# Performance work log

Hardware: AMD Instinct MI355X
Metric: run time of the kernel (lower is better)

The kernel has to match this reference:

```python
import jax, jax.numpy as jnp
import numpy as np

N_NODES = 100000


def setup_inputs() -> dict:
    key = jax.random.key(0)
    k1, k2, k3, k4, k5 = jax.random.split(key, 5)
    features = jax.random.normal(k1, (N_NODES, 512), dtype=jnp.float32)
    edge_src = jax.random.randint(k2, (640000,), 0, N_NODES, dtype=jnp.int64)
    edge_dst = jax.random.randint(k3, (640000,), 0, N_NODES, dtype=jnp.int64)
    edge_weight = jax.random.uniform(k4, (640000,), dtype=jnp.float32)
    weights = jax.random.normal(k5, (512, 128), dtype=jnp.float32) * (2.0 / 512) ** 0.5  # kaiming-ish scale
    bias = jnp.zeros((128,), dtype=jnp.float32)
    return {
        "features": features,
        "edge_src": edge_src,
        "edge_dst": edge_dst,
        "edge_weight": edge_weight,
        "weights": weights,
        "bias": bias,
    }


def reference(features, edge_src, edge_dst, edge_weight, weights, bias):
    # X' = A @ (X @ W) + b, with sparse A given as COO edges (src -> dst).
    h = jnp.matmul(features, weights)                      # [N, d_out] dense GEMM
    msg = edge_weight[:, None] * h[edge_src]               # [E, d_out] gather + scale
    out = jax.ops.segment_sum(msg, edge_dst, num_segments=N_NODES)  # sparse aggregation
    return out + bias
```

## Files before the change

### kernel.cpp

```cpp
#include <hip/hip_runtime.h>


#define D_IN  512
#define D_OUT 128
#define CAP   32

typedef __attribute__((ext_vector_type(8))) short short8;
typedef __attribute__((ext_vector_type(4))) float f32x4;
typedef __attribute__((ext_vector_type(4))) int i32x4;
typedef __attribute__((ext_vector_type(8))) unsigned short u16x8;
typedef __attribute__((ext_vector_type(2))) unsigned long long u64x2;

static __device__ __forceinline__ unsigned short f2bf(float f) {
    unsigned u = __float_as_uint(f);
    unsigned r = (u + 0x7FFFu + ((u >> 16) & 1u)) >> 16;
    return (unsigned short)r;
}

static __device__ __forceinline__ int pack2(float lo, float hi) {
    return (int)((__float_as_uint(hi) & 0xFFFF0000u) | (__float_as_uint(lo) >> 16));
}

__global__ __launch_bounds__(256) void prep_kernel(const float* __restrict__ W,
                                                   unsigned short* __restrict__ Wt,
                                                   int* __restrict__ deg,
                                                   unsigned long long* __restrict__ bucket,
                                                   int M) {
    int t = blockIdx.x * 256 + threadIdx.x;
    if (t < D_OUT * D_IN) {
        int n = t >> 9;
        int k = t & 511;
        Wt[t] = f2bf(W[(size_t)k * D_OUT + n]);
    }
    if (t < M) deg[t] = 0;
    const int stride = gridDim.x * 256;
    const int npair = M * (CAP / 2);
    u64x2 z = {0ull, 0ull};
    for (int i = t; i < npair; i += stride)
        __builtin_nontemporal_store(z, reinterpret_cast<u64x2*>(bucket) + i);
}

__global__ __launch_bounds__(256, 2) void gemm_build_kernel(
        const float* __restrict__ X, const unsigned short* __restrict__ Wt,
        unsigned short* __restrict__ H, int M,
        const int* __restrict__ src, const int* __restrict__ dst,
        const float* __restrict__ w, int* __restrict__ deg,
        unsigned long long* __restrict__ bucket, int E, int nG) {
    if ((int)blockIdx.x >= nG) {
        int e = ((int)blockIdx.x - nG) * 256 + threadIdx.x;
        if (e < E) {
            int d = dst[e];
            int pos = atomicAdd(&deg[d], 1);
            if (pos < CAP)
                bucket[(size_t)d * CAP + pos] =
                    ((unsigned long long)__float_as_uint(w[e]) << 32) | (unsigned)src[e];
        }
        return;
    }

    const int tid = threadIdx.x;
    const int lane = tid & 63;
    const int wv = tid >> 6;
    const int block_row = blockIdx.x * 128;

    const int m = lane & 15;
    const int q = lane >> 4;
    const int wave_row = wv * 32;

    const float* Xr[2];
#pragma unroll
    for (int rg = 0; rg < 2; rg++) {
        int grow = block_row + wave_row + rg * 16 + m;
        if (grow >= M) grow = M - 1;
        Xr[rg] = X + (size_t)grow * D_IN;
    }
    const unsigned short* Wn[8];
#pragma unroll
    for (int cg = 0; cg < 8; cg++) Wn[cg] = Wt + (size_t)(cg * 16 + m) * D_IN;

    f32x4 acc[2][8];
#pragma unroll
    for (int a = 0; a < 2; a++)
#pragma unroll
        for (int b = 0; b < 8; b++) acc[a][b] = (f32x4){0.f, 0.f, 0.f, 0.f};

    f32x4 Ab[3][2][2];
    short8 Bb[2][8];

#define KB(ks) ((ks) * 32 + q * 8)
#define LOAD_A(st, ks)                                                         \
    do {                                                                       \
        _Pragma("unroll") for (int rg = 0; rg < 2; rg++) {                     \
            Ab[st][rg][0] = *reinterpret_cast<const f32x4*>(Xr[rg] + KB(ks));  \
            Ab[st][rg][1] = *reinterpret_cast<const f32x4*>(Xr[rg] + KB(ks) + 4); \
        }                                                                      \
    } while (0)
#define LOAD_B(st, ks)                                                         \
    do {                                                                       \
        _Pragma("unroll") for (int cg = 0; cg < 8; cg++)                       \
            Bb[st][cg] = *reinterpret_cast<const short8*>(Wn[cg] + KB(ks));    \
    } while (0)

    LOAD_A(0, 0);
    LOAD_A(1, 1);
    LOAD_A(2, 2);
    LOAD_B(0, 0);
    LOAD_B(1, 1);

#pragma unroll
    for (int ks = 0; ks < 16; ks++) {
        const int sA = ks % 3;
        const int sB = ks % 2;
        short8 afr[2];
#pragma unroll
        for (int rg = 0; rg < 2; rg++) {
            f32x4 u0 = Ab[sA][rg][0];
            f32x4 u1 = Ab[sA][rg][1];
            i32x4 ai;
            ai.x = pack2(u0.x, u0.y);
            ai.y = pack2(u0.z, u0.w);
            ai.z = pack2(u1.x, u1.y);
            ai.w = pack2(u1.z, u1.w);
            afr[rg] = __builtin_bit_cast(short8, ai);
        }
        if (ks + 3 < 16) LOAD_A(sA, ks + 3);
#pragma unroll
        for (int rg = 0; rg < 2; rg++)
#pragma unroll
            for (int cg = 0; cg < 8; cg++)
                acc[rg][cg] = __builtin_amdgcn_mfma_f32_16x16x32_bf16(
                    afr[rg], Bb[sB][cg], acc[rg][cg], 0, 0, 0);
        if (ks + 2 < 16) LOAD_B(sB, ks + 2);
    }
#undef KB
#undef LOAD_A
#undef LOAD_B

#pragma unroll
    for (int rg = 0; rg < 2; rg++) {
#pragma unroll
        for (int r = 0; r < 4; r++) {
            int grow = block_row + wave_row + rg * 16 + q * 4 + r;
            if (grow < M) {
#pragma unroll
                for (int cg = 0; cg < 8; cg++)
                    H[(size_t)grow * D_OUT + cg * 16 + m] = f2bf(acc[rg][cg][r]);
            }
        }
    }
}

__global__ __launch_bounds__(256) void agg_kernel(const unsigned short* __restrict__ H,
                                                  const int* __restrict__ deg,
                                                  const unsigned long long* __restrict__ bucket,
                                                  const float* __restrict__ bias,
                                                  float* __restrict__ out, int M) {
    int row = blockIdx.x * 16 + (threadIdx.x >> 4);
    if (row >= M) return;
    int sub = threadIdx.x & 15;

    f32x4 b0 = *reinterpret_cast<const f32x4*>(bias + sub * 8);
    f32x4 b1 = *reinterpret_cast<const f32x4*>(bias + sub * 8 + 4);
    float acc[8] = {b0.x, b0.y, b0.z, b0.w, b1.x, b1.y, b1.z, b1.w};

    int n = deg[row];
    if (n > CAP) n = CAP;
    const unsigned long long* bp = bucket + (size_t)row * CAP;

    for (int j = 0; j < n; j += 4) {
        u64x2 q0 = __builtin_nontemporal_load(reinterpret_cast<const u64x2*>(bp + j));
        u64x2 q1 = __builtin_nontemporal_load(reinterpret_cast<const u64x2*>(bp + j + 2));
        unsigned long long p0 = q0[0];
        unsigned long long p1 = q0[1];
        unsigned long long p2 = q1[0];
        unsigned long long p3 = q1[1];
        u16x8 v0 = *reinterpret_cast<const u16x8*>(
            H + (size_t)(unsigned)(p0 & 0xFFFFFFFFull) * D_OUT + sub * 8);
        u16x8 v1 = *reinterpret_cast<const u16x8*>(
            H + (size_t)(unsigned)(p1 & 0xFFFFFFFFull) * D_OUT + sub * 8);
        u16x8 v2 = *reinterpret_cast<const u16x8*>(
            H + (size_t)(unsigned)(p2 & 0xFFFFFFFFull) * D_OUT + sub * 8);
        u16x8 v3 = *reinterpret_cast<const u16x8*>(
            H + (size_t)(unsigned)(p3 & 0xFFFFFFFFull) * D_OUT + sub * 8);
        float w0 = __uint_as_float((unsigned)(p0 >> 32));
        float w1 = __uint_as_float((unsigned)(p1 >> 32));
        float w2 = __uint_as_float((unsigned)(p2 >> 32));
        float w3 = __uint_as_float((unsigned)(p3 >> 32));
#pragma unroll
        for (int c = 0; c < 8; c++) {
            acc[c] += w0 * __uint_as_float((unsigned)v0[c] << 16);
            acc[c] += w1 * __uint_as_float((unsigned)v1[c] << 16);
            acc[c] += w2 * __uint_as_float((unsigned)v2[c] << 16);
            acc[c] += w3 * __uint_as_float((unsigned)v3[c] << 16);
        }
    }

    f32x4 o0 = {acc[0], acc[1], acc[2], acc[3]};
    f32x4 o1 = {acc[4], acc[5], acc[6], acc[7]};
    __builtin_nontemporal_store(o0, reinterpret_cast<f32x4*>(out + (size_t)row * D_OUT + sub * 8));
    __builtin_nontemporal_store(o1, reinterpret_cast<f32x4*>(out + (size_t)row * D_OUT + sub * 8 + 4));
}

extern "C" void kernel_launch(void* const* d_in, const int* in_sizes, int n_in,
                              void* d_out, int out_size, void* d_ws, size_t ws_size,
                              hipStream_t stream) {
    const float* features    = (const float*)d_in[0];
    const int*   edge_src    = (const int*)d_in[1];
    const int*   edge_dst    = (const int*)d_in[2];
    const float* edge_weight = (const float*)d_in[3];
    const float* weights     = (const float*)d_in[4];
    const float* bias        = (const float*)d_in[5];
    float* out = (float*)d_out;

    const int M = in_sizes[0] / D_IN;
    const int E = in_sizes[1];

    char* ws = (char*)d_ws;
    unsigned short* hbf = (unsigned short*)(ws);
    unsigned short* Wt  = (unsigned short*)(ws + 25600000);
    int* deg            = (int*)(ws + 25731072);
    unsigned long long* bucket = (unsigned long long*)(ws + 26131456);

    int mx = (M > D_OUT * D_IN) ? M : (D_OUT * D_IN);
    prep_kernel<<<(mx + 255) / 256, 256, 0, stream>>>(weights, Wt, deg, bucket, M);

    const int nG = (M + 127) / 128;
    const int nB = (E + 255) / 256;
    gemm_build_kernel<<<nG + nB, 256, 0, stream>>>(features, Wt, hbf, M,
                                                   edge_src, edge_dst, edge_weight,
                                                   deg, bucket, E, nG);

    agg_kernel<<<(M + 15) / 16, 256, 0, stream>>>(hbf, deg, bucket, bias, out, M);
}
```

Before: 411.7 us.

## Stage GEMM tiles through LDS with async global_load_lds and unroll aggregation by 8

The GEMM now stages 128x32 fp32 X tiles and 128x32 bf16 W tiles into double-buffered, XOR-swizzled shared memory using direct global-to-LDS loads. Waves are arranged as a 2x2 grid of 64x64 output tiles, so W is no longer read separately by every wave straight from global memory. The launch bound occupancy hint rises from 2 to 3. The aggregation loop now processes 8 bucket entries per iteration instead of 4, issuing more independent gathers at once. This relies on the zero-filled bucket padding, since rows with a degree that is not a multiple of 8 read up to 7 extra padded slots.

```diff
diff --git a/kernel.cpp b/kernel.cpp
--- a/kernel.cpp
+++ b/kernel.cpp
@@ -10,6 +10,9 @@
 typedef __attribute__((ext_vector_type(4))) int i32x4;
 typedef __attribute__((ext_vector_type(8))) unsigned short u16x8;
 typedef __attribute__((ext_vector_type(2))) unsigned long long u64x2;
+
+typedef __attribute__((address_space(1))) const unsigned int glob_u32;
+typedef __attribute__((address_space(3))) unsigned int lds_u32;
 
 static __device__ __forceinline__ unsigned short f2bf(float f) {
     unsigned u = __float_as_uint(f);
@@ -40,12 +43,15 @@
         __builtin_nontemporal_store(z, reinterpret_cast<u64x2*>(bucket) + i);
 }
 
-__global__ __launch_bounds__(256, 2) void gemm_build_kernel(
+__global__ __launch_bounds__(256, 3) void gemm_build_kernel(
         const float* __restrict__ X, const unsigned short* __restrict__ Wt,
         unsigned short* __restrict__ H, int M,
         const int* __restrict__ src, const int* __restrict__ dst,
         const float* __restrict__ w, int* __restrict__ deg,
         unsigned long long* __restrict__ bucket, int E, int nG) {
+    __shared__ float As[2 * 128 * 32];
+    __shared__ unsigned short Bs[2 * 128 * 32];
+
     if ((int)blockIdx.x >= nG) {
         int e = ((int)blockIdx.x - nG) * 256 + threadIdx.x;
         if (e < E) {
@@ -65,86 +71,113 @@
 
     const int m = lane & 15;
     const int q = lane >> 4;
-    const int wave_row = wv * 32;
-
-    const float* Xr[2];
-#pragma unroll
-    for (int rg = 0; rg < 2; rg++) {
-        int grow = block_row + wave_row + rg * 16 + m;
-        if (grow >= M) grow = M - 1;
-        Xr[rg] = X + (size_t)grow * D_IN;
-    }
-    const unsigned short* Wn[8];
-#pragma unroll
-    for (int cg = 0; cg < 8; cg++) Wn[cg] = Wt + (size_t)(cg * 16 + m) * D_IN;
-
-    f32x4 acc[2][8];
-#pragma unroll
-    for (int a = 0; a < 2; a++)
-#pragma unroll
-        for (int b = 0; b < 8; b++) acc[a][b] = (f32x4){0.f, 0.f, 0.f, 0.f};
-
-    f32x4 Ab[3][2][2];
-    short8 Bb[2][8];
-
-#define KB(ks) ((ks) * 32 + q * 8)
-#define LOAD_A(st, ks)                                                         \
+    const int wave_row = (wv >> 1) * 64;
+    const int wave_col = (wv & 1) * 64;
+
+    f32x4 acc[4][4];
+#pragma unroll
+    for (int a = 0; a < 4; a++)
+#pragma unroll
+        for (int b = 0; b < 4; b++) acc[a][b] = (f32x4){0.f, 0.f, 0.f, 0.f};
+
+#define STAGE(BUF, T)                                                          \
     do {                                                                       \
-        _Pragma("unroll") for (int rg = 0; rg < 2; rg++) {                     \
-            Ab[st][rg][0] = *reinterpret_cast<const f32x4*>(Xr[rg] + KB(ks));  \
-            Ab[st][rg][1] = *reinterpret_cast<const f32x4*>(Xr[rg] + KB(ks) + 4); \
+        const int kc_ = (T) * 32;                                              \
+        _Pragma("unroll") for (int it = 0; it < 4; it++) {                     \
+            int slot_base = wv * 256 + it * 64;              \
+            int s = slot_base + lane;                                          \
+            int row = s >> 3;                                                  \
+            int kq = (s & 7) ^ (row & 7);                                      \
+            int grow = block_row + row;                                        \
+            if (grow >= M) grow = M - 1;                                       \
+            const float* gp = X + (size_t)grow * D_IN + kc_ + kq * 4;          \
+            __builtin_amdgcn_global_load_lds((glob_u32*)gp,                    \
+                (lds_u32*)(As + (BUF) * 4096 + (size_t)slot_base * 4), 16, 0, 0); \
+        }                                                                      \
+        _Pragma("unroll") for (int it = 0; it < 2; it++) {                     \
+            int slot_base = wv * 128 + it * 64;                                \
+            int s = slot_base + lane;                                          \
+            int n = s >> 2;                                                    \
+            int kq = (s & 3) ^ (n & 3);                                        \
+            const unsigned short* gp = Wt + (size_t)n * D_IN + kc_ + kq * 8;   \
+            __builtin_amdgcn_global_load_lds((glob_u32*)gp,                    \
+                (lds_u32*)(Bs + (BUF) * 4096 + (size_t)slot_base * 8), 16, 0, 0); \
         }                                                                      \
     } while (0)
-#define LOAD_B(st, ks)                                                         \
+
+#define COMPUTE(BUF)                                                           \
     do {                                                                       \
-        _Pragma("unroll") for (int cg = 0; cg < 8; cg++)                       \
-            Bb[st][cg] = *reinterpret_cast<const short8*>(Wn[cg] + KB(ks));    \
+        const float* Ap = As + (BUF) * 4096;                                   \
+        const unsigned short* Bp = Bs + (BUF) * 4096;                          \
+        short8 afr[4];                                                         \
+        _Pragma("unroll") for (int rg = 0; rg < 4; rg++) {                     \
+            int row = wave_row + rg * 16 + m;                                  \
+            int kq0 = 2 * q;                                                   \
+            f32x4 u0 = *reinterpret_cast<const f32x4*>(                        \
+                Ap + (size_t)(row * 8 + (kq0 ^ (row & 7))) * 4);               \
+            f32x4 u1 = *reinterpret_cast<const f32x4*>(                        \
+                Ap + (size_t)(row * 8 + ((kq0 + 1) ^ (row & 7))) * 4);         \
+            i32x4 ai;                                                          \
+            ai.x = pack2(u0.x, u0.y);                                          \
+            ai.y = pack2(u0.z, u0.w);                                          \
+            ai.z = pack2(u1.x, u1.y);                                          \
+            ai.w = pack2(u1.z, u1.w);                                          \
+            afr[rg] = __builtin_bit_cast(short8, ai);                          \
+        }                                                                      \
+        short8 bfr[4];                                                         \
+        _Pragma("unroll") for (int cg = 0; cg < 4; cg++) {                     \
+            int n = wave_col + cg * 16 + m;                                    \
+            bfr[cg] = *reinterpret_cast<const short8*>(                        \
+                Bp + (size_t)(n * 4 + (q ^ (n & 3))) * 8);                     \
+        }                                                                      \
+        _Pragma("unroll") for (int rg = 0; rg < 4; rg++)                       \
+            _Pragma("unroll") for (int cg = 0; cg < 4; cg++)                   \
+                acc[rg][cg] = __builtin_amdgcn_mfma_f32_16x16x32_bf16(         \
+                    afr[rg], bfr[cg], acc[rg][cg], 0, 0, 0);                   \
     } while (0)
 
-    LOAD_A(0, 0);
-    LOAD_A(1, 1);
-    LOAD_A(2, 2);
-    LOAD_B(0, 0);
-    LOAD_B(1, 1);
-
-#pragma unroll
-    for (int ks = 0; ks < 16; ks++) {
-        const int sA = ks % 3;
-        const int sB = ks % 2;
-        short8 afr[2];
-#pragma unroll
-        for (int rg = 0; rg < 2; rg++) {
-            f32x4 u0 = Ab[sA][rg][0];
-            f32x4 u1 = Ab[sA][rg][1];
-            i32x4 ai;
-            ai.x = pack2(u0.x, u0.y);
-            ai.y = pack2(u0.z, u0.w);
-            ai.z = pack2(u1.x, u1.y);
-            ai.w = pack2(u1.z, u1.w);
-            afr[rg] = __builtin_bit_cast(short8, ai);
-        }
-        if (ks + 3 < 16) LOAD_A(sA, ks + 3);
-#pragma unroll
-        for (int rg = 0; rg < 2; rg++)
-#pragma unroll
-            for (int cg = 0; cg < 8; cg++)
-                acc[rg][cg] = __builtin_amdgcn_mfma_f32_16x16x32_bf16(
-                    afr[rg], Bb[sB][cg], acc[rg][cg], 0, 0, 0);
-        if (ks + 2 < 16) LOAD_B(sB, ks + 2);
-    }
-#undef KB
-#undef LOAD_A
-#undef LOAD_B
-
-#pragma unroll
-    for (int rg = 0; rg < 2; rg++) {
+#define STEP(BUF, T, VMS)                                                      \
+    do {                                                                       \
+        if ((T) + 1 < 16) STAGE((BUF) ^ 1, (T) + 1);                           \
+        asm volatile("s_waitcnt vmcnt(" VMS ")" ::: "memory");                 \
+        __builtin_amdgcn_s_barrier();                                          \
+        asm volatile("" ::: "memory");     \
+        COMPUTE(BUF);                                                          \
+        __builtin_amdgcn_s_barrier();                                          \
+        asm volatile("" ::: "memory");                                         \
+    } while (0)
+
+    STAGE(0, 0);
+    STEP(0, 0, "6");
+    STEP(1, 1, "6");
+    STEP(0, 2, "6");
+    STEP(1, 3, "6");
+    STEP(0, 4, "6");
+    STEP(1, 5, "6");
+    STEP(0, 6, "6");
+    STEP(1, 7, "6");
+    STEP(0, 8, "6");
+    STEP(1, 9, "6");
+    STEP(0, 10, "6");
+    STEP(1, 11, "6");
+    STEP(0, 12, "6");
+    STEP(1, 13, "6");
+    STEP(0, 14, "6");
+    STEP(1, 15, "0");
+
+#undef STAGE
+#undef COMPUTE
+#undef STEP
+
+#pragma unroll
+    for (int rg = 0; rg < 4; rg++) {
 #pragma unroll
         for (int r = 0; r < 4; r++) {
             int grow = block_row + wave_row + rg * 16 + q * 4 + r;
             if (grow < M) {
 #pragma unroll
-                for (int cg = 0; cg < 8; cg++)
-                    H[(size_t)grow * D_OUT + cg * 16 + m] = f2bf(acc[rg][cg][r]);
+                for (int cg = 0; cg < 4; cg++)
+                    H[(size_t)grow * D_OUT + wave_col + cg * 16 + m] = f2bf(acc[rg][cg][r]);
             }
         }
     }
@@ -167,31 +200,23 @@
     if (n > CAP) n = CAP;
     const unsigned long long* bp = bucket + (size_t)row * CAP;
 
-    for (int j = 0; j < n; j += 4) {
+    for (int j = 0; j < n; j += 8) {
         u64x2 q0 = __builtin_nontemporal_load(reinterpret_cast<const u64x2*>(bp + j));
         u64x2 q1 = __builtin_nontemporal_load(reinterpret_cast<const u64x2*>(bp + j + 2));
-        unsigned long long p0 = q0[0];
-        unsigned long long p1 = q0[1];
-        unsigned long long p2 = q1[0];
-        unsigned long long p3 = q1[1];
-        u16x8 v0 = *reinterpret_cast<const u16x8*>(
-            H + (size_t)(unsigned)(p0 & 0xFFFFFFFFull) * D_OUT + sub * 8);
-        u16x8 v1 = *reinterpret_cast<const u16x8*>(
-            H + (size_t)(unsigned)(p1 & 0xFFFFFFFFull) * D_OUT + sub * 8);
-        u16x8 v2 = *reinterpret_cast<const u16x8*>(
-            H + (size_t)(unsigned)(p2 & 0xFFFFFFFFull) * D_OUT + sub * 8);
-        u16x8 v3 = *reinterpret_cast<const u16x8*>(
-            H + (size_t)(unsigned)(p3 & 0xFFFFFFFFull) * D_OUT + sub * 8);
-        float w0 = __uint_as_float((unsigned)(p0 >> 32));
-        float w1 = __uint_as_float((unsigned)(p1 >> 32));
-        float w2 = __uint_as_float((unsigned)(p2 >> 32));
-        float w3 = __uint_as_float((unsigned)(p3 >> 32));
-#pragma unroll
-        for (int c = 0; c < 8; c++) {
-            acc[c] += w0 * __uint_as_float((unsigned)v0[c] << 16);
-            acc[c] += w1 * __uint_as_float((unsigned)v1[c] << 16);
-            acc[c] += w2 * __uint_as_float((unsigned)v2[c] << 16);
-            acc[c] += w3 * __uint_as_float((unsigned)v3[c] << 16);
+        u64x2 q2 = __builtin_nontemporal_load(reinterpret_cast<const u64x2*>(bp + j + 4));
+        u64x2 q3 = __builtin_nontemporal_load(reinterpret_cast<const u64x2*>(bp + j + 6));
+        unsigned long long p[8] = {q0[0], q0[1], q1[0], q1[1], q2[0], q2[1], q3[0], q3[1]};
+        u16x8 v[8];
+#pragma unroll
+        for (int i = 0; i < 8; i++)
+            v[i] = *reinterpret_cast<const u16x8*>(
+                H + (size_t)(unsigned)(p[i] & 0xFFFFFFFFull) * D_OUT + sub * 8);
+#pragma unroll
+        for (int i = 0; i < 8; i++) {
+            float wi = __uint_as_float((unsigned)(p[i] >> 32));
+#pragma unroll
+            for (int c = 0; c < 8; c++)
+                acc[c] += wi * __uint_as_float((unsigned)v[i][c] << 16);
         }
     }
 
```

After: 380.6 us. -7.6%, faster.
